# Performance work log

Hardware: AMD Instinct MI355X
Metric: run time of the kernel (lower is better)

The kernel has to match this reference:

```python
import jax, jax.numpy as jnp
import numpy as np

NUM_LAYERS = 3  # min_num_layers == max_num_layers == 3 (deterministic stochastic depth)
LN_EPS = 1e-5


def setup_inputs() -> dict:
    key = jax.random.key(0)
    k1, k2, k3 = jax.random.split(key, 3)
    N, d, F = 8, 16, 512  # (batch, in_dim=out_dim, num_features)
    x = jax.random.normal(k1, (N, d, F), dtype=jnp.float32)
    W = jax.random.normal(k2, (d, F, F, d), dtype=jnp.float32)  # recurrent weight
    A = jax.random.uniform(k3, (2, F, F), dtype=jnp.float32)    # transition mats, steps 1..2
    return {"x": x, "W": W, "A": A}


def _contract(h, W, a):
    # h: (N,d,F), W: (d,F,F,o), a: (F,F) -> (N,o,F)
    # Equivalent to (h.unsqueeze(-1).unsqueeze(-1) * (W * a[...,None])).sum(1).sum(1).transpose(1,2)
    return jnp.einsum('ndf,dfgo,fg->nog', h, W, a)


def _layer_norm(y):
    # torch applies layer_norm over the channel dim (axis 1 of (N,o,F)), no affine params
    m = y.mean(axis=1, keepdims=True)
    v = y.var(axis=1, keepdims=True)
    return (y - m) / jnp.sqrt(v + LN_EPS)


def reference(x, W, A):
    history = [x]
    for i in range(1, NUM_LAYERS):
        # recurrent + residual branch: average contributions from all previous layers
        ys = [_contract(history[j], W, A[i - j - 1]) for j in range(i)]
        y = jnp.mean(jnp.stack(ys, axis=0), axis=0)
        y = _layer_norm(y)
        history.append(y)
    return history[-1]  # return_layers='last'
```

## Files before the change

### kernel.cpp

```cpp
#include <hip/hip_runtime.h>
#include <stdint.h>


#define F_CHUNK 32
#define N_CHUNKS 16

__global__ void k0_prep_x(const float* __restrict__ x, float* __restrict__ xT) {
    int idx = blockIdx.x * blockDim.x + threadIdx.x;
    int n = idx & 7, d = (idx >> 3) & 15, f = idx >> 7;
    xT[idx] = x[n * 8192 + d * 512 + f];
}

template <bool PASS_A>
__global__ __launch_bounds__(256)
void k_contract(const float* __restrict__ W, const float* __restrict__ A,
                const float* __restrict__ xT,
                float* __restrict__ p0, float* __restrict__ p1) {
    const int t  = threadIdx.x;
    const int fc = blockIdx.x;
    const int ct = blockIdx.y;
    const int g  = ct * 16 + (t >> 4);
    const int o  = t & 15;
    const int col = g * 16 + o;
    const int f0 = fc * F_CHUNK;

    float c0[8], c1[8];
#pragma unroll
    for (int n = 0; n < 8; ++n) { c0[n] = 0.f; c1[n] = 0.f; }

    const float* Wc = W + col;
    for (int f = f0; f < f0 + F_CHUNK; ++f) {
        float w[16];
#pragma unroll
        for (int d = 0; d < 16; ++d)
            w[d] = Wc[(size_t)d * 4194304 + (size_t)f * 8192];

        const float* xf = xT + f * 128;
        float p[8];
#pragma unroll
        for (int n = 0; n < 8; ++n) p[n] = 0.f;
#pragma unroll
        for (int d = 0; d < 16; ++d) {
#pragma unroll
            for (int n = 0; n < 8; ++n)
                p[n] = fmaf(xf[d * 8 + n], w[d], p[n]);
        }

        float a0 = A[f * 512 + g];
#pragma unroll
        for (int n = 0; n < 8; ++n) c0[n] = fmaf(a0, p[n], c0[n]);
        if constexpr (PASS_A) {
            float a1 = A[262144 + f * 512 + g];
#pragma unroll
            for (int n = 0; n < 8; ++n) c1[n] = fmaf(a1, p[n], c1[n]);
        }
    }

    size_t base = (((size_t)fc * 512 + g) * 16 + o) * 8;
#pragma unroll
    for (int n = 0; n < 8; ++n) p0[base + n] = c0[n];
    if constexpr (PASS_A) {
#pragma unroll
        for (int n = 0; n < 8; ++n) p1[base + n] = c1[n];
    }
}

__global__ __launch_bounds__(128)
void k_reduce_ln(const float* __restrict__ part, float* __restrict__ outT) {
    __shared__ float sh[16][8];
    int g = blockIdx.x;
    int t = threadIdx.x;
    int o = t >> 3, n = t & 7;
    float s = 0.f;
    for (int ch = 0; ch < 16; ++ch)
        s += part[(((size_t)ch * 512 + g) * 16 + o) * 8 + n];
    sh[o][n] = s;
    __syncthreads();
    float m = 0.f, v = 0.f;
#pragma unroll
    for (int oo = 0; oo < 16; ++oo) { float y = sh[oo][n]; m += y; v += y * y; }
    m *= (1.f / 16.f);
    v = v * (1.f / 16.f) - m * m;
    float r = rsqrtf(v + 1e-5f);
    outT[((size_t)g * 16 + o) * 8 + n] = (s - m) * r;
}

__global__ __launch_bounds__(128)
void k_final(const float* __restrict__ p1, const float* __restrict__ p2,
             float* __restrict__ out) {
    __shared__ float sh[16][8];
    int g = blockIdx.x;
    int t = threadIdx.x;
    int o = t >> 3, n = t & 7;
    float s = 0.f;
    for (int ch = 0; ch < 16; ++ch) {
        size_t idx = (((size_t)ch * 512 + g) * 16 + o) * 8 + n;
        s += p1[idx] + p2[idx];
    }
    s *= 0.5f;
    sh[o][n] = s;
    __syncthreads();
    float m = 0.f, v = 0.f;
#pragma unroll
    for (int oo = 0; oo < 16; ++oo) { float y = sh[oo][n]; m += y; v += y * y; }
    m *= (1.f / 16.f);
    v = v * (1.f / 16.f) - m * m;
    float r = rsqrtf(v + 1e-5f);
    out[n * 8192 + o * 512 + g] = (s - m) * r;
}

extern "C" void kernel_launch(void* const* d_in, const int* in_sizes, int n_in,
                              void* d_out, int out_size, void* d_ws, size_t ws_size,
                              hipStream_t stream) {
    const float* x = (const float*)d_in[0];
    const float* W = (const float*)d_in[1];
    const float* A = (const float*)d_in[2];
    float* out = (float*)d_out;

    float* ws  = (float*)d_ws;
    float* xT  = ws;
    float* xT2 = ws + 65536;
    float* c0p = ws + 131072;
    float* c1p = c0p + 1048576;
    float* c2p = c1p + 1048576;

    k0_prep_x<<<256, 256, 0, stream>>>(x, xT);
    k_contract<true ><<<dim3(N_CHUNKS, 32), 256, 0, stream>>>(W, A, xT,  c0p, c1p);
    k_reduce_ln<<<512, 128, 0, stream>>>(c0p, xT2);
    k_contract<false><<<dim3(N_CHUNKS, 32), 256, 0, stream>>>(W, A, xT2, c2p, nullptr);
    k_final<<<512, 128, 0, stream>>>(c1p, c2p, out);
}
```

Baseline: 428.2 us.

## Compute two output columns per thread with float2 W loads and finer F chunks

Each contraction thread now handles two adjacent (g,o) columns, loading W as float2 so every x value read from xT feeds two FMAs. The F dimension is split into 32 chunks of 16 instead of 16 chunks of 32, so the grid keeps the same block count while the column tiles halve. The partial buffers are re-laid out and doubled in size, and the reduce kernels loop over more chunks. The x transpose kernel is also changed to read x coalesced and scatter its writes. In exchange, register pressure roughly doubles (launch bounds now ask for 2 blocks) and the partial-sum traffic grows.

```diff
diff --git a/kernel.cpp b/kernel.cpp
--- a/kernel.cpp
+++ b/kernel.cpp
@@ -2,66 +2,74 @@
 #include <stdint.h>
 
 
-#define F_CHUNK 32
-#define N_CHUNKS 16
+#define F_CHUNK 16
+#define N_CHUNKS 32
 
 __global__ void k0_prep_x(const float* __restrict__ x, float* __restrict__ xT) {
     int idx = blockIdx.x * blockDim.x + threadIdx.x;
-    int n = idx & 7, d = (idx >> 3) & 15, f = idx >> 7;
-    xT[idx] = x[n * 8192 + d * 512 + f];
+    int f = idx & 511, d = (idx >> 9) & 15, n = idx >> 13;
+    xT[f * 128 + d * 8 + n] = x[idx];
 }
 
 template <bool PASS_A>
-__global__ __launch_bounds__(256)
+__global__ __launch_bounds__(256, 2)
 void k_contract(const float* __restrict__ W, const float* __restrict__ A,
                 const float* __restrict__ xT,
                 float* __restrict__ p0, float* __restrict__ p1) {
     const int t  = threadIdx.x;
     const int fc = blockIdx.x;
     const int ct = blockIdx.y;
-    const int g  = ct * 16 + (t >> 4);
-    const int o  = t & 15;
-    const int col = g * 16 + o;
+    const int col = ct * 512 + t * 2;
+    const int g  = col >> 4;
     const int f0 = fc * F_CHUNK;
 
-    float c0[8], c1[8];
+    float c00[8], c01[8], c10[8], c11[8];
 #pragma unroll
-    for (int n = 0; n < 8; ++n) { c0[n] = 0.f; c1[n] = 0.f; }
+    for (int n = 0; n < 8; ++n) { c00[n] = 0.f; c01[n] = 0.f; c10[n] = 0.f; c11[n] = 0.f; }
 
     const float* Wc = W + col;
     for (int f = f0; f < f0 + F_CHUNK; ++f) {
-        float w[16];
+        float2 w[16];
 #pragma unroll
         for (int d = 0; d < 16; ++d)
-            w[d] = Wc[(size_t)d * 4194304 + (size_t)f * 8192];
+            w[d] = *(const float2*)(Wc + (size_t)d * 4194304 + (size_t)f * 8192);
 
         const float* xf = xT + f * 128;
-        float p[8];
+        float pa[8], pb[8];
 #pragma unroll
-        for (int n = 0; n < 8; ++n) p[n] = 0.f;
+        for (int n = 0; n < 8; ++n) { pa[n] = 0.f; pb[n] = 0.f; }
 #pragma unroll
         for (int d = 0; d < 16; ++d) {
 #pragma unroll
-            for (int n = 0; n < 8; ++n)
-                p[n] = fmaf(xf[d * 8 + n], w[d], p[n]);
+            for (int n = 0; n < 8; ++n) {
+                float xv = xf[d * 8 + n];
+                pa[n] = fmaf(xv, w[d].x, pa[n]);
+                pb[n] = fmaf(xv, w[d].y, pb[n]);
+            }
         }
 
         float a0 = A[f * 512 + g];
 #pragma unroll
-        for (int n = 0; n < 8; ++n) c0[n] = fmaf(a0, p[n], c0[n]);
+        for (int n = 0; n < 8; ++n) {
+            c00[n] = fmaf(a0, pa[n], c00[n]);
+            c01[n] = fmaf(a0, pb[n], c01[n]);
+        }
         if constexpr (PASS_A) {
             float a1 = A[262144 + f * 512 + g];
 #pragma unroll
-            for (int n = 0; n < 8; ++n) c1[n] = fmaf(a1, p[n], c1[n]);
+            for (int n = 0; n < 8; ++n) {
+                c10[n] = fmaf(a1, pa[n], c10[n]);
+                c11[n] = fmaf(a1, pb[n], c11[n]);
+            }
         }
     }
 
-    size_t base = (((size_t)fc * 512 + g) * 16 + o) * 8;
+    size_t base = (((size_t)fc * 8192 + col)) * 8;
 #pragma unroll
-    for (int n = 0; n < 8; ++n) p0[base + n] = c0[n];
+    for (int n = 0; n < 8; ++n) { p0[base + n] = c00[n]; p0[base + 8 + n] = c01[n]; }
     if constexpr (PASS_A) {
 #pragma unroll
-        for (int n = 0; n < 8; ++n) p1[base + n] = c1[n];
+        for (int n = 0; n < 8; ++n) { p1[base + n] = c10[n]; p1[base + 8 + n] = c11[n]; }
     }
 }
 
@@ -72,8 +80,8 @@
     int t = threadIdx.x;
     int o = t >> 3, n = t & 7;
     float s = 0.f;
-    for (int ch = 0; ch < 16; ++ch)
-        s += part[(((size_t)ch * 512 + g) * 16 + o) * 8 + n];
+    for (int ch = 0; ch < N_CHUNKS; ++ch)
+        s += part[((size_t)ch * 8192 + g * 16 + o) * 8 + n];
     sh[o][n] = s;
     __syncthreads();
     float m = 0.f, v = 0.f;
@@ -93,8 +101,8 @@
     int t = threadIdx.x;
     int o = t >> 3, n = t & 7;
     float s = 0.f;
-    for (int ch = 0; ch < 16; ++ch) {
-        size_t idx = (((size_t)ch * 512 + g) * 16 + o) * 8 + n;
+    for (int ch = 0; ch < N_CHUNKS; ++ch) {
+        size_t idx = ((size_t)ch * 8192 + g * 16 + o) * 8 + n;
         s += p1[idx] + p2[idx];
     }
     s *= 0.5f;
@@ -121,12 +129,12 @@
     float* xT  = ws;
     float* xT2 = ws + 65536;
     float* c0p = ws + 131072;
-    float* c1p = c0p + 1048576;
-    float* c2p = c1p + 1048576;
+    float* c1p = c0p + 2097152;
+    float* c2p = c1p + 2097152;
 
     k0_prep_x<<<256, 256, 0, stream>>>(x, xT);
-    k_contract<true ><<<dim3(N_CHUNKS, 32), 256, 0, stream>>>(W, A, xT,  c0p, c1p);
+    k_contract<true ><<<dim3(N_CHUNKS, 16), 256, 0, stream>>>(W, A, xT,  c0p, c1p);
     k_reduce_ln<<<512, 128, 0, stream>>>(c0p, xT2);
-    k_contract<false><<<dim3(N_CHUNKS, 32), 256, 0, stream>>>(W, A, xT2, c2p, nullptr);
+    k_contract<false><<<dim3(N_CHUNKS, 16), 256, 0, stream>>>(W, A, xT2, c2p, nullptr);
     k_final<<<512, 128, 0, stream>>>(c1p, c2p, out);
 }
```

After: 436.2 us. About the same (+1.9%).
